# Kernel optimization log

Hardware: AMD Instinct MI355X
Metric: run time of the kernel (lower is better)

The kernel has to match this reference:

```python
import jax, jax.numpy as jnp
import numpy as np

N_NODES = 10000
N_EDGES = 160000
EMBED = 512
RBF = 64
ANG = 16


def setup_inputs() -> dict:
    key = jax.random.key(0)
    ks = jax.random.split(key, 12)
    x = jax.random.normal(ks[0], (N_NODES, EMBED), dtype=jnp.float32)
    coord = jax.random.normal(ks[1], (N_NODES, 3), dtype=jnp.float32)
    edge_index = jax.random.randint(ks[2], (2, N_EDGES), 0, N_NODES, dtype=jnp.int64)
    rbf_feature = jax.random.normal(ks[3], (N_EDGES, RBF), dtype=jnp.float32)
    angle_feature = jax.random.normal(ks[4], (N_EDGES, ANG), dtype=jnp.float32)
    s = 1.0 / np.sqrt(RBF + ANG)
    W_edge = jax.random.normal(ks[5], (RBF + ANG, EMBED), dtype=jnp.float32) * s
    b_edge = jax.random.normal(ks[6], (EMBED,), dtype=jnp.float32) * 0.01
    s2 = 1.0 / np.sqrt(EMBED)
    W1 = jax.random.normal(ks[7], (EMBED, EMBED), dtype=jnp.float32) * s2
    b1 = jax.random.normal(ks[8], (EMBED,), dtype=jnp.float32) * 0.01
    W2 = jax.random.normal(ks[9], (EMBED, EMBED), dtype=jnp.float32) * s2
    b2 = jax.random.normal(ks[10], (EMBED,), dtype=jnp.float32) * 0.01
    return {"x": x, "coord": coord, "edge_index": edge_index,
            "rbf_feature": rbf_feature, "angle_feature": angle_feature,
            "W_edge": W_edge, "b_edge": b_edge,
            "W1": W1, "b1": b1, "W2": W2, "b2": b2}


def reference(x, coord, edge_index, rbf_feature, angle_feature,
              W_edge, b_edge, W1, b1, W2, b2):
    row = edge_index[0]  # destination nodes for scatter-add
    edge_feat = jnp.concatenate([rbf_feature, angle_feature], axis=-1)  # [E, 80]
    msg = edge_feat @ W_edge + b_edge                                    # [E, D]
    agg = jax.ops.segment_sum(msg, row, num_segments=x.shape[0])         # [N, D]
    h = jax.nn.relu(agg @ W1 + b1) @ W2 + b2                             # node MLP
    return x + h
```

## Files before the change

### kernel.cpp

```cpp
#include <hip/hip_runtime.h>

constexpr int NN = 10000;
constexpr int NE = 160000;
constexpr int D  = 512;
constexpr int KC = 8;
constexpr int MAXDEG = 96;

typedef __attribute__((ext_vector_type(8))) short short8;
typedef __attribute__((ext_vector_type(4))) float f32x4;

static __device__ __forceinline__ ushort f2bf(float f) {
    union { float f; unsigned u; } v; v.f = f;
    unsigned r = (v.u + 0x7FFFu + ((v.u >> 16) & 1u)) >> 16;
    return (ushort)r;
}

typedef __attribute__((address_space(3))) unsigned int lds_uint;
typedef const __attribute__((address_space(1))) unsigned int glb_uint;
static __device__ __forceinline__ void gload16(const ushort* g, ushort* l) {
    __builtin_amdgcn_global_load_lds((glb_uint*)g, (lds_uint*)l, 16, 0, 0);
}

__global__ __launch_bounds__(256)
void prep1_kernel(const float* __restrict__ We,
                  const float* __restrict__ be,
                  const float* __restrict__ W1,
                  const float* __restrict__ W2,
                  float* __restrict__ part,
                  ushort* __restrict__ W2t,
                  int* __restrict__ deg) {
    __shared__ float tile[32][33];
    const int b   = blockIdx.x;
    const int tid = threadIdx.x;

    if (b < 1344) {
        const int c  = (b & 7) * 64 + (tid & 63);
        const int r  = ((b >> 3) % 21) * 4 + (tid >> 6);
        const int kc = b / 168;
        if (r > 80) return;
        const float* arow = (r < 80) ? (We + (size_t)r * D) : be;
        const int k0 = kc * 64;
        float s = 0.f;
        #pragma unroll
        for (int k = 0; k < 64; k += 4) {
            float4 a = *reinterpret_cast<const float4*>(&arow[k0 + k]);
            s += a.x * W1[(size_t)(k0 + k    ) * D + c];
            s += a.y * W1[(size_t)(k0 + k + 1) * D + c];
            s += a.z * W1[(size_t)(k0 + k + 2) * D + c];
            s += a.w * W1[(size_t)(k0 + k + 3) * D + c];
        }
        part[((size_t)kc * 81 + r) * D + c] = s;
    } else if (b < 1600) {
        const int t  = b - 1344;
        const int bx = (t & 15) * 32;
        const int by = (t >> 4) * 32;
        const int tx = tid & 31;
        const int ty = tid >> 5;
        #pragma unroll
        for (int i = 0; i < 4; ++i)
            tile[ty + 8 * i][tx] = W2[(size_t)(by + ty + 8 * i) * D + bx + tx];
        __syncthreads();
        #pragma unroll
        for (int i = 0; i < 4; ++i)
            W2t[(size_t)(bx + ty + 8 * i) * D + by + tx] = f2bf(tile[tx][ty + 8 * i]);
    } else {
        const int i = (b - 1600) * 256 + tid;
        if (i < NN) deg[i] = 0;
    }
}

__global__ __launch_bounds__(256)
void prep2_kernel(const float* __restrict__ part,
                  const int* __restrict__ row,
                  ushort* __restrict__ WcT,
                  int* __restrict__ deg,
                  int* __restrict__ ell) {
    const int b   = blockIdx.x;
    const int tid = threadIdx.x;
    if (b < 256) {
        const int i = b * 256 + tid;
        const int k = i >> 9;
        const int c = i & 511;
        float s = 0.f;
        if (k <= 80) {
            #pragma unroll
            for (int kc = 0; kc < KC; ++kc)
                s += part[((size_t)kc * 81 + k) * D + c];
        }
        WcT[(size_t)c * 128 + k] = f2bf(s);
    } else {
        const int e = (b - 256) * 256 + tid;
        if (e < NE) {
            int r = row[e];
            int slot = atomicAdd(&deg[r], 1);
            if (slot < MAXDEG) ell[r * MAXDEG + slot] = e;
        }
    }
}

__global__ __launch_bounds__(256)
void gather_agg_kernel(const int* __restrict__ deg,
                       const int* __restrict__ ell,
                       const float* __restrict__ rbf,
                       const float* __restrict__ ang,
                       ushort* __restrict__ aggX) {
    const int wv   = threadIdx.x >> 6;
    const int lane = threadIdx.x & 63;
    const int n    = blockIdx.x * 4 + wv;
    if (n >= NN) return;
    int d = deg[n];
    if (d > MAXDEG) d = MAXDEG;
    const int* en = ell + (size_t)n * MAXDEG;
    float s1 = 0.f, s2 = 0.f;
    int i = 0;
    for (; i + 8 <= d; i += 8) {
        int e[8];
        #pragma unroll
        for (int j = 0; j < 8; ++j) e[j] = en[i + j];
        float v[8];
        #pragma unroll
        for (int j = 0; j < 8; ++j) v[j] = rbf[e[j] * 64 + lane];
        if (lane < 16) {
            #pragma unroll
            for (int j = 0; j < 8; ++j) s2 += ang[e[j] * 16 + lane];
        }
        #pragma unroll
        for (int j = 0; j < 8; ++j) s1 += v[j];
    }
    for (; i + 4 <= d; i += 4) {
        const int e0 = en[i], e1 = en[i + 1], e2 = en[i + 2], e3 = en[i + 3];
        const float v0 = rbf[e0 * 64 + lane];
        const float v1 = rbf[e1 * 64 + lane];
        const float v2 = rbf[e2 * 64 + lane];
        const float v3 = rbf[e3 * 64 + lane];
        if (lane < 16) {
            s2 += ang[e0 * 16 + lane] + ang[e1 * 16 + lane]
                + ang[e2 * 16 + lane] + ang[e3 * 16 + lane];
        }
        s1 += v0 + v1 + v2 + v3;
    }
    for (; i < d; ++i) {
        const int e = en[i];
        s1 += rbf[e * 64 + lane];
        if (lane < 16) s2 += ang[e * 16 + lane];
    }
    aggX[(size_t)n * 128 + lane] = f2bf(s1);
    const float v2 = (lane < 16) ? s2 : (lane == 16 ? (float)d : 0.f);
    aggX[(size_t)n * 128 + 64 + lane] = f2bf(v2);
}

__global__ __launch_bounds__(256)
void h1_mfma_kernel(const ushort* __restrict__ A,
                    const ushort* __restrict__ Bt,
                    const float* __restrict__ b1,
                    ushort* __restrict__ H, int M) {
    __shared__ ushort As[128 * 128];
    __shared__ ushort Bs[64 * 128];
    const int tid  = threadIdx.x;
    const int lane = tid & 63;
    const int wid  = tid >> 6;

    const int l = blockIdx.y * gridDim.x + blockIdx.x;
    const int cpx = (gridDim.x * gridDim.y) >> 3;
    const int t_ = (l & 7) * cpx + (l >> 3);
    const int n0 = (t_ & 7) * 64;
    const int m0 = (t_ >> 3) * 128;

    const int rg = lane >> 4;
    const int ch = lane & 15;

    f32x4 acc[2][4] = {};

    #pragma unroll
    for (int j = 0; j < 8; ++j) {
        const int r  = wid * 32 + j * 4 + rg;
        const int gm = (m0 + r < M) ? (m0 + r) : (M - 1);
        const int cs = (ch ^ (r & 7)) * 8;
        const int rowbase = wid * 32 + j * 4;
        gload16(A + (size_t)gm * 128 + cs, &As[rowbase * 128]);
    }
    #pragma unroll
    for (int j = 0; j < 4; ++j) {
        const int r  = wid * 16 + j * 4 + rg;
        const int cs = (ch ^ (r & 7)) * 8;
        const int rowbase = wid * 16 + j * 4;
        gload16(Bt + (size_t)(n0 + r) * 128 + cs, &Bs[rowbase * 128]);
    }
    __syncthreads();

    #pragma unroll
    for (int kk = 0; kk < 4; ++kk) {
        const int kc = kk * 4 + (lane >> 4);
        short8 af[2], bfr[4];
        #pragma unroll
        for (int mf = 0; mf < 2; ++mf) {
            const int ar = wid * 32 + mf * 16 + (lane & 15);
            af[mf] = *reinterpret_cast<const short8*>(
                &As[ar * 128 + ((kc ^ (ar & 7)) * 8)]);
        }
        #pragma unroll
        for (int nf = 0; nf < 4; ++nf) {
            const int br = nf * 16 + (lane & 15);
            bfr[nf] = *reinterpret_cast<const short8*>(
                &Bs[br * 128 + ((kc ^ (br & 7)) * 8)]);
        }
        #pragma unroll
        for (int mf = 0; mf < 2; ++mf)
            #pragma unroll
            for (int nf = 0; nf < 4; ++nf)
                acc[mf][nf] = __builtin_amdgcn_mfma_f32_16x16x32_bf16(
                    af[mf], bfr[nf], acc[mf][nf], 0, 0, 0);
    }

    #pragma unroll
    for (int mf = 0; mf < 2; ++mf) {
        const int rowb = m0 + wid * 32 + mf * 16 + ((lane >> 4) << 2);
        #pragma unroll
        for (int nf = 0; nf < 4; ++nf) {
            const int col = n0 + nf * 16 + (lane & 15);
            const float bv = b1[col];
            #pragma unroll
            for (int r = 0; r < 4; ++r) {
                const int row = rowb + r;
                if (row < M)
                    H[(size_t)row * D + col] = f2bf(fmaxf(acc[mf][nf][r] + bv, 0.f));
            }
        }
    }
}

__global__ __launch_bounds__(256)
void mfma_gemm_kernel(const ushort* __restrict__ A,
                      const ushort* __restrict__ Bt,
                      const float* __restrict__ bias,
                      const float* __restrict__ xres,
                      float* __restrict__ Cout, int M) {
    __shared__ ushort As[2][128 * 64];
    __shared__ ushort Bs[2][64 * 64];
    const int tid  = threadIdx.x;
    const int lane = tid & 63;
    const int wid  = tid >> 6;

    const int l = blockIdx.y * gridDim.x + blockIdx.x;
    const int cpx = (gridDim.x * gridDim.y) >> 3;
    const int t_ = (l & 7) * cpx + (l >> 3);
    const int n0 = (t_ & 7) * 64;
    const int m0 = (t_ >> 3) * 128;

    const int sr = lane >> 3;
    const int sc = lane & 7;

    f32x4 acc[2][4] = {};
    constexpr int KTILES = D / 64;

    auto stage = [&](int buf, int t) {
        #pragma unroll
        for (int j = 0; j < 4; ++j) {
            const int r  = wid * 32 + j * 8 + sr;
            const int gm = (m0 + r < M) ? (m0 + r) : (M - 1);
            const int cs = (sc ^ (r & 7)) * 8;
            const int rowbase = wid * 32 + j * 8;
            gload16(A + (size_t)gm * D + t * 64 + cs, &As[buf][rowbase * 64]);
        }
        #pragma unroll
        for (int j = 0; j < 2; ++j) {
            const int r  = wid * 16 + j * 8 + sr;
            const int cs = (sc ^ (r & 7)) * 8;
            const int rowbase = wid * 16 + j * 8;
            gload16(Bt + (size_t)(n0 + r) * D + t * 64 + cs, &Bs[buf][rowbase * 64]);
        }
    };

    stage(0, 0);
    __syncthreads();

    for (int t = 0; t < KTILES; ++t) {
        const int cur = t & 1;
        if (t + 1 < KTILES) stage(cur ^ 1, t + 1);
        #pragma unroll
        for (int kk = 0; kk < 2; ++kk) {
            const int kc = kk * 4 + (lane >> 4);
            short8 af[2], bfr[4];
            #pragma unroll
            for (int mf = 0; mf < 2; ++mf) {
                const int ar = wid * 32 + mf * 16 + (lane & 15);
                af[mf] = *reinterpret_cast<const short8*>(
                    &As[cur][ar * 64 + ((kc ^ (ar & 7)) * 8)]);
            }
            #pragma unroll
            for (int nf = 0; nf < 4; ++nf) {
                const int br = nf * 16 + (lane & 15);
                bfr[nf] = *reinterpret_cast<const short8*>(
                    &Bs[cur][br * 64 + ((kc ^ (br & 7)) * 8)]);
            }
            #pragma unroll
            for (int mf = 0; mf < 2; ++mf)
                #pragma unroll
                for (int nf = 0; nf < 4; ++nf)
                    acc[mf][nf] = __builtin_amdgcn_mfma_f32_16x16x32_bf16(
                        af[mf], bfr[nf], acc[mf][nf], 0, 0, 0);
        }
        __syncthreads();
    }

    #pragma unroll
    for (int mf = 0; mf < 2; ++mf) {
        const int rowb = m0 + wid * 32 + mf * 16 + ((lane >> 4) << 2);
        #pragma unroll
        for (int nf = 0; nf < 4; ++nf) {
            const int col = n0 + nf * 16 + (lane & 15);
            const float bv = bias[col];
            #pragma unroll
            for (int r = 0; r < 4; ++r) {
                const int row = rowb + r;
                if (row < M)
                    Cout[(size_t)row * D + col] =
                        acc[mf][nf][r] + bv + xres[(size_t)row * D + col];
            }
        }
    }
}

extern "C" void kernel_launch(void* const* d_in, const int* in_sizes, int n_in,
                              void* d_out, int out_size, void* d_ws, size_t ws_size,
                              hipStream_t stream) {
    const float* x      = (const float*)d_in[0];
    const int*   edge_index = (const int*)d_in[2];
    const float* rbf    = (const float*)d_in[3];
    const float* ang    = (const float*)d_in[4];
    const float* W_edge = (const float*)d_in[5];
    const float* b_edge = (const float*)d_in[6];
    const float* W1     = (const float*)d_in[7];
    const float* b1     = (const float*)d_in[8];
    const float* W2     = (const float*)d_in[9];
    const float* b2     = (const float*)d_in[10];
    float* out = (float*)d_out;

    char* w = (char*)d_ws;
    ushort* aggX = (ushort*)w;
    ushort* W2t  = (ushort*)(w + 2560000);
    ushort* WcT  = (ushort*)(w + 3084288);
    int*    deg  = (int*)(w + 3215360);
    float*  part = (float*)(w + 3255360);
    int*    ell  = (int*)(w + 4582464);
    ushort* h1   = (ushort*)(w + 3255360);

    prep1_kernel<<<1640, 256, 0, stream>>>(W_edge, b_edge, W1, W2, part, W2t, deg);
    prep2_kernel<<<881, 256, 0, stream>>>(part, edge_index, WcT, deg, ell);
    gather_agg_kernel<<<NN / 4, 256, 0, stream>>>(deg, ell, rbf, ang, aggX);

    dim3 ggrid(D / 64, (NN + 127) / 128);
    h1_mfma_kernel<<<ggrid, 256, 0, stream>>>(aggX, WcT, b1, h1, NN);
    mfma_gemm_kernel<<<ggrid, 256, 0, stream>>>(h1, W2t, b2, x, out, NN);
}
```

Measured before the change: 70.58 us.

## Fuse gather and both node GEMMs into one cooperative kernel with grid syncs

Replaces the three launches (gather aggregation, first MFMA GEMM, second MFMA GEMM) with a single cooperative kernel of 632 blocks that uses grid-wide syncs between phases. The aim is to cut kernel launch gaps and tail effects between the dependent stages. In exchange, it depends on cooperative launch succeeding with all 632 blocks resident, and it adds grid-sync costs. It keeps the old multi-kernel path as a fallback if the cooperative launch fails.

```diff
diff --git a/kernel.cpp b/kernel.cpp
--- a/kernel.cpp
+++ b/kernel.cpp
@@ -1,4 +1,7 @@
 #include <hip/hip_runtime.h>
+#include <hip/hip_cooperative_groups.h>
+
+namespace cg = cooperative_groups;
 
 constexpr int NN = 10000;
 constexpr int NE = 160000;
@@ -22,12 +25,9 @@
 }
 
 __global__ __launch_bounds__(256)
-void prep1_kernel(const float* __restrict__ We,
-                  const float* __restrict__ be,
-                  const float* __restrict__ W1,
-                  const float* __restrict__ W2,
-                  float* __restrict__ part,
-                  ushort* __restrict__ W2t,
+void prep1_kernel(const float* __restrict__ We, const float* __restrict__ be,
+                  const float* __restrict__ W1, const float* __restrict__ W2,
+                  float* __restrict__ part, ushort* __restrict__ W2t,
                   int* __restrict__ deg) {
     __shared__ float tile[32][33];
     const int b   = blockIdx.x;
@@ -70,10 +70,8 @@
 }
 
 __global__ __launch_bounds__(256)
-void prep2_kernel(const float* __restrict__ part,
-                  const int* __restrict__ row,
-                  ushort* __restrict__ WcT,
-                  int* __restrict__ deg,
+void prep2_kernel(const float* __restrict__ part, const int* __restrict__ row,
+                  ushort* __restrict__ WcT, int* __restrict__ deg,
                   int* __restrict__ ell) {
     const int b   = blockIdx.x;
     const int tid = threadIdx.x;
@@ -98,16 +96,11 @@
     }
 }
 
-__global__ __launch_bounds__(256)
-void gather_agg_kernel(const int* __restrict__ deg,
-                       const int* __restrict__ ell,
-                       const float* __restrict__ rbf,
-                       const float* __restrict__ ang,
-                       ushort* __restrict__ aggX) {
-    const int wv   = threadIdx.x >> 6;
-    const int lane = threadIdx.x & 63;
-    const int n    = blockIdx.x * 4 + wv;
-    if (n >= NN) return;
+static __device__ __forceinline__ void gather_body(
+        int n, int lane,
+        const int* __restrict__ deg, const int* __restrict__ ell,
+        const float* __restrict__ rbf, const float* __restrict__ ang,
+        ushort* __restrict__ aggX) {
     int d = deg[n];
     if (d > MAXDEG) d = MAXDEG;
     const int* en = ell + (size_t)n * MAXDEG;
@@ -149,11 +142,191 @@
     aggX[(size_t)n * 128 + 64 + lane] = f2bf(v2);
 }
 
+__global__ __launch_bounds__(256, 3)
+void fused_kernel(const int* __restrict__ deg, const int* __restrict__ ell,
+                  const float* __restrict__ rbf, const float* __restrict__ ang,
+                  ushort* __restrict__ aggX, const ushort* __restrict__ WcT,
+                  const float* __restrict__ b1, ushort* __restrict__ h1,
+                  const ushort* __restrict__ W2t, const float* __restrict__ b2,
+                  const float* __restrict__ x, float* __restrict__ out) {
+    __shared__ ushort smem[24576];
+    cg::grid_group grid = cg::this_grid();
+
+    const int tid  = threadIdx.x;
+    const int lane = tid & 63;
+    const int wid  = tid >> 6;
+
+    for (int g = blockIdx.x; g < NN / 4; g += gridDim.x)
+        gather_body(g * 4 + wid, lane, deg, ell, rbf, ang, aggX);
+    grid.sync();
+
+    const int l = blockIdx.x;
+    const int cpx = gridDim.x >> 3;
+    const int t_ = (l & 7) * cpx + (l >> 3);
+    const int n0 = (t_ & 7) * 64;
+    const int m0 = (t_ >> 3) * 128;
+    constexpr int M = NN;
+
+    {
+        ushort* As = smem;
+        ushort* Bs = smem + 16384;
+        const int rg = lane >> 4;
+        const int ch = lane & 15;
+
+        f32x4 acc[2][4] = {};
+
+        #pragma unroll
+        for (int j = 0; j < 8; ++j) {
+            const int r  = wid * 32 + j * 4 + rg;
+            const int gm = (m0 + r < M) ? (m0 + r) : (M - 1);
+            const int cs = (ch ^ (r & 7)) * 8;
+            const int rowbase = wid * 32 + j * 4;
+            gload16(aggX + (size_t)gm * 128 + cs, &As[rowbase * 128]);
+        }
+        #pragma unroll
+        for (int j = 0; j < 4; ++j) {
+            const int r  = wid * 16 + j * 4 + rg;
+            const int cs = (ch ^ (r & 7)) * 8;
+            const int rowbase = wid * 16 + j * 4;
+            gload16(WcT + (size_t)(n0 + r) * 128 + cs, &Bs[rowbase * 128]);
+        }
+        __syncthreads();
+
+        #pragma unroll
+        for (int kk = 0; kk < 4; ++kk) {
+            const int kc = kk * 4 + (lane >> 4);
+            short8 af[2], bfr[4];
+            #pragma unroll
+            for (int mf = 0; mf < 2; ++mf) {
+                const int ar = wid * 32 + mf * 16 + (lane & 15);
+                af[mf] = *reinterpret_cast<const short8*>(
+                    &As[ar * 128 + ((kc ^ (ar & 7)) * 8)]);
+            }
+            #pragma unroll
+            for (int nf = 0; nf < 4; ++nf) {
+                const int br = nf * 16 + (lane & 15);
+                bfr[nf] = *reinterpret_cast<const short8*>(
+                    &Bs[br * 128 + ((kc ^ (br & 7)) * 8)]);
+            }
+            #pragma unroll
+            for (int mf = 0; mf < 2; ++mf)
+                #pragma unroll
+                for (int nf = 0; nf < 4; ++nf)
+                    acc[mf][nf] = __builtin_amdgcn_mfma_f32_16x16x32_bf16(
+                        af[mf], bfr[nf], acc[mf][nf], 0, 0, 0);
+        }
+
+        #pragma unroll
+        for (int mf = 0; mf < 2; ++mf) {
+            const int rowb = m0 + wid * 32 + mf * 16 + ((lane >> 4) << 2);
+            #pragma unroll
+            for (int nf = 0; nf < 4; ++nf) {
+                const int col = n0 + nf * 16 + (lane & 15);
+                const float bv = b1[col];
+                #pragma unroll
+                for (int r = 0; r < 4; ++r) {
+                    const int row = rowb + r;
+                    if (row < M)
+                        h1[(size_t)row * D + col] =
+                            f2bf(fmaxf(acc[mf][nf][r] + bv, 0.f));
+                }
+            }
+        }
+    }
+    __syncthreads();
+    grid.sync();
+
+    {
+        ushort* As0 = smem;
+        ushort* Bs0 = smem + 16384;
+        const int sr = lane >> 3;
+        const int sc = lane & 7;
+
+        f32x4 acc[2][4] = {};
+        constexpr int KTILES = D / 64;
+
+        auto stage = [&](int buf, int t) {
+            #pragma unroll
+            for (int j = 0; j < 4; ++j) {
+                const int r  = wid * 32 + j * 8 + sr;
+                const int gm = (m0 + r < M) ? (m0 + r) : (M - 1);
+                const int cs = (sc ^ (r & 7)) * 8;
+                const int rowbase = wid * 32 + j * 8;
+                gload16(h1 + (size_t)gm * D + t * 64 + cs,
+                        &As0[buf * 8192 + rowbase * 64]);
+            }
+            #pragma unroll
+            for (int j = 0; j < 2; ++j) {
+                const int r  = wid * 16 + j * 8 + sr;
+                const int cs = (sc ^ (r & 7)) * 8;
+                const int rowbase = wid * 16 + j * 8;
+                gload16(W2t + (size_t)(n0 + r) * D + t * 64 + cs,
+                        &Bs0[buf * 4096 + rowbase * 64]);
+            }
+        };
+
+        stage(0, 0);
+        __syncthreads();
+
+        for (int t = 0; t < KTILES; ++t) {
+            const int cur = t & 1;
+            if (t + 1 < KTILES) stage(cur ^ 1, t + 1);
+            #pragma unroll
+            for (int kk = 0; kk < 2; ++kk) {
+                const int kc = kk * 4 + (lane >> 4);
+                short8 af[2], bfr[4];
+                #pragma unroll
+                for (int mf = 0; mf < 2; ++mf) {
+                    const int ar = wid * 32 + mf * 16 + (lane & 15);
+                    af[mf] = *reinterpret_cast<const short8*>(
+                        &As0[cur * 8192 + ar * 64 + ((kc ^ (ar & 7)) * 8)]);
+                }
+                #pragma unroll
+                for (int nf = 0; nf < 4; ++nf) {
+                    const int br = nf * 16 + (lane & 15);
+                    bfr[nf] = *reinterpret_cast<const short8*>(
+                        &Bs0[cur * 4096 + br * 64 + ((kc ^ (br & 7)) * 8)]);
+                }
+                #pragma unroll
+                for (int mf = 0; mf < 2; ++mf)
+                    #pragma unroll
+                    for (int nf = 0; nf < 4; ++nf)
+                        acc[mf][nf] = __builtin_amdgcn_mfma_f32_16x16x32_bf16(
+                            af[mf], bfr[nf], acc[mf][nf], 0, 0, 0);
+            }
+            __syncthreads();
+        }
+
+        #pragma unroll
+        for (int mf = 0; mf < 2; ++mf) {
+            const int rowb = m0 + wid * 32 + mf * 16 + ((lane >> 4) << 2);
+            #pragma unroll
+            for (int nf = 0; nf < 4; ++nf) {
+                const int col = n0 + nf * 16 + (lane & 15);
+                const float bv = b2[col];
+                #pragma unroll
+                for (int r = 0; r < 4; ++r) {
+                    const int row = rowb + r;
+                    if (row < M)
+                        out[(size_t)row * D + col] =
+                            acc[mf][nf][r] + bv + x[(size_t)row * D + col];
+                }
+            }
+        }
+    }
+}
+
 __global__ __launch_bounds__(256)
-void h1_mfma_kernel(const ushort* __restrict__ A,
-                    const ushort* __restrict__ Bt,
-                    const float* __restrict__ b1,
-                    ushort* __restrict__ H, int M) {
+void gather_agg_kernel(const int* __restrict__ deg, const int* __restrict__ ell,
+                       const float* __restrict__ rbf, const float* __restrict__ ang,
+                       ushort* __restrict__ aggX) {
+    const int n = blockIdx.x * 4 + (threadIdx.x >> 6);
+    if (n < NN) gather_body(n, threadIdx.x & 63, deg, ell, rbf, ang, aggX);
+}
+
+__global__ __launch_bounds__(256)
+void h1_mfma_kernel(const ushort* __restrict__ A, const ushort* __restrict__ Bt,
+                    const float* __restrict__ b1, ushort* __restrict__ H, int M) {
     __shared__ ushort As[128 * 128];
     __shared__ ushort Bs[64 * 128];
     const int tid  = threadIdx.x;
@@ -230,10 +403,8 @@
 }
 
 __global__ __launch_bounds__(256)
-void mfma_gemm_kernel(const ushort* __restrict__ A,
-                      const ushort* __restrict__ Bt,
-                      const float* __restrict__ bias,
-                      const float* __restrict__ xres,
+void mfma_gemm_kernel(const ushort* __restrict__ A, const ushort* __restrict__ Bt,
+                      const float* __restrict__ bias, const float* __restrict__ xres,
                       float* __restrict__ Cout, int M) {
     __shared__ ushort As[2][128 * 64];
     __shared__ ushort Bs[2][64 * 64];
@@ -347,9 +518,20 @@
 
     prep1_kernel<<<1640, 256, 0, stream>>>(W_edge, b_edge, W1, W2, part, W2t, deg);
     prep2_kernel<<<881, 256, 0, stream>>>(part, edge_index, WcT, deg, ell);
-    gather_agg_kernel<<<NN / 4, 256, 0, stream>>>(deg, ell, rbf, ang, aggX);
-
-    dim3 ggrid(D / 64, (NN + 127) / 128);
-    h1_mfma_kernel<<<ggrid, 256, 0, stream>>>(aggX, WcT, b1, h1, NN);
-    mfma_gemm_kernel<<<ggrid, 256, 0, stream>>>(h1, W2t, b2, x, out, NN);
-}
+
+    const int* degc = deg;
+    const int* ellc = ell;
+    const ushort* WcTc = WcT;
+    const ushort* W2tc = W2t;
+    void* args[] = {(void*)&degc, (void*)&ellc, (void*)&rbf, (void*)&ang,
+                    (void*)&aggX, (void*)&WcTc, (void*)&b1, (void*)&h1,
+                    (void*)&W2tc, (void*)&b2, (void*)&x, (void*)&out};
+    hipError_t err = hipLaunchCooperativeKernel((void*)fused_kernel, dim3(632),
+                                                dim3(256), args, 0, stream);
+    if (err != hipSuccess) {
+        gather_agg_kernel<<<NN / 4, 256, 0, stream>>>(deg, ell, rbf, ang, aggX);
+        dim3 ggrid(D / 64, (NN + 127) / 128);
+        h1_mfma_kernel<<<ggrid, 256, 0, stream>>>(aggX, WcT, b1, h1, NN);
+        mfma_gemm_kernel<<<ggrid, 256, 0, stream>>>(h1, W2t, b2, x, out, NN);
+    }
+}
```

Result: slower. 219.6 us (+211.1%).

## Fuse node MLP GEMMs into one kernel, recomputing hidden tile per block

Applied to the files above, without the earlier changes.

Merges the h1 GEMM and the second GEMM into a single tail kernel. Each block computes a 128x64 slice of relu(agg@Wc+b1) in registers and LDS for every K-tile, then immediately multiplies it by the matching W2 slice. This removes the bf16 h1 round trip through global memory and one kernel launch. In exchange, every one of the 8 column blocks recomputes the full hidden tile, so the first GEMM's compute is repeated 8 times.

```diff
diff --git a/kernel.cpp b/kernel.cpp
--- a/kernel.cpp
+++ b/kernel.cpp
@@ -22,12 +22,9 @@
 }
 
 __global__ __launch_bounds__(256)
-void prep1_kernel(const float* __restrict__ We,
-                  const float* __restrict__ be,
-                  const float* __restrict__ W1,
-                  const float* __restrict__ W2,
-                  float* __restrict__ part,
-                  ushort* __restrict__ W2t,
+void prep1_kernel(const float* __restrict__ We, const float* __restrict__ be,
+                  const float* __restrict__ W1, const float* __restrict__ W2,
+                  float* __restrict__ part, ushort* __restrict__ W2t,
                   int* __restrict__ deg) {
     __shared__ float tile[32][33];
     const int b   = blockIdx.x;
@@ -70,10 +67,8 @@
 }
 
 __global__ __launch_bounds__(256)
-void prep2_kernel(const float* __restrict__ part,
-                  const int* __restrict__ row,
-                  ushort* __restrict__ WcT,
-                  int* __restrict__ deg,
+void prep2_kernel(const float* __restrict__ part, const int* __restrict__ row,
+                  ushort* __restrict__ WcT, int* __restrict__ deg,
                   int* __restrict__ ell) {
     const int b   = blockIdx.x;
     const int tid = threadIdx.x;
@@ -99,10 +94,8 @@
 }
 
 __global__ __launch_bounds__(256)
-void gather_agg_kernel(const int* __restrict__ deg,
-                       const int* __restrict__ ell,
-                       const float* __restrict__ rbf,
-                       const float* __restrict__ ang,
+void gather_agg_kernel(const int* __restrict__ deg, const int* __restrict__ ell,
+                       const float* __restrict__ rbf, const float* __restrict__ ang,
                        ushort* __restrict__ aggX) {
     const int wv   = threadIdx.x >> 6;
     const int lane = threadIdx.x & 63;
@@ -150,12 +143,16 @@
 }
 
 __global__ __launch_bounds__(256)
-void h1_mfma_kernel(const ushort* __restrict__ A,
-                    const ushort* __restrict__ Bt,
-                    const float* __restrict__ b1,
-                    ushort* __restrict__ H, int M) {
-    __shared__ ushort As[128 * 128];
-    __shared__ ushort Bs[64 * 128];
+void tail_kernel(const ushort* __restrict__ aggX,
+                 const ushort* __restrict__ WcT,
+                 const float* __restrict__ b1,
+                 const ushort* __restrict__ W2t,
+                 const float* __restrict__ b2,
+                 const float* __restrict__ x,
+                 float* __restrict__ out, int M) {
+    __shared__ ushort Wc_s[2][64 * 128];
+    __shared__ ushort W2_s[2][64 * 64];
+    __shared__ ushort Ah[128 * 64];
     const int tid  = threadIdx.x;
     const int lane = tid & 63;
     const int wid  = tid >> 6;
@@ -166,117 +163,87 @@
     const int n0 = (t_ & 7) * 64;
     const int m0 = (t_ >> 3) * 128;
 
-    const int rg = lane >> 4;
-    const int ch = lane & 15;
-
-    f32x4 acc[2][4] = {};
-
-    #pragma unroll
-    for (int j = 0; j < 8; ++j) {
-        const int r  = wid * 32 + j * 4 + rg;
-        const int gm = (m0 + r < M) ? (m0 + r) : (M - 1);
-        const int cs = (ch ^ (r & 7)) * 8;
-        const int rowbase = wid * 32 + j * 4;
-        gload16(A + (size_t)gm * 128 + cs, &As[rowbase * 128]);
-    }
-    #pragma unroll
-    for (int j = 0; j < 4; ++j) {
-        const int r  = wid * 16 + j * 4 + rg;
-        const int cs = (ch ^ (r & 7)) * 8;
-        const int rowbase = wid * 16 + j * 4;
-        gload16(Bt + (size_t)(n0 + r) * 128 + cs, &Bs[rowbase * 128]);
-    }
-    __syncthreads();
-
-    #pragma unroll
-    for (int kk = 0; kk < 4; ++kk) {
-        const int kc = kk * 4 + (lane >> 4);
-        short8 af[2], bfr[4];
-        #pragma unroll
-        for (int mf = 0; mf < 2; ++mf) {
-            const int ar = wid * 32 + mf * 16 + (lane & 15);
-            af[mf] = *reinterpret_cast<const short8*>(
-                &As[ar * 128 + ((kc ^ (ar & 7)) * 8)]);
-        }
-        #pragma unroll
-        for (int nf = 0; nf < 4; ++nf) {
-            const int br = nf * 16 + (lane & 15);
-            bfr[nf] = *reinterpret_cast<const short8*>(
-                &Bs[br * 128 + ((kc ^ (br & 7)) * 8)]);
-        }
-        #pragma unroll
-        for (int mf = 0; mf < 2; ++mf)
-            #pragma unroll
-            for (int nf = 0; nf < 4; ++nf)
-                acc[mf][nf] = __builtin_amdgcn_mfma_f32_16x16x32_bf16(
-                    af[mf], bfr[nf], acc[mf][nf], 0, 0, 0);
-    }
-
+    short8 afh[2][4];
     #pragma unroll
     for (int mf = 0; mf < 2; ++mf) {
-        const int rowb = m0 + wid * 32 + mf * 16 + ((lane >> 4) << 2);
-        #pragma unroll
-        for (int nf = 0; nf < 4; ++nf) {
-            const int col = n0 + nf * 16 + (lane & 15);
-            const float bv = b1[col];
-            #pragma unroll
-            for (int r = 0; r < 4; ++r) {
-                const int row = rowb + r;
-                if (row < M)
-                    H[(size_t)row * D + col] = f2bf(fmaxf(acc[mf][nf][r] + bv, 0.f));
-            }
-        }
-    }
-}
-
-__global__ __launch_bounds__(256)
-void mfma_gemm_kernel(const ushort* __restrict__ A,
-                      const ushort* __restrict__ Bt,
-                      const float* __restrict__ bias,
-                      const float* __restrict__ xres,
-                      float* __restrict__ Cout, int M) {
-    __shared__ ushort As[2][128 * 64];
-    __shared__ ushort Bs[2][64 * 64];
-    const int tid  = threadIdx.x;
-    const int lane = tid & 63;
-    const int wid  = tid >> 6;
-
-    const int l = blockIdx.y * gridDim.x + blockIdx.x;
-    const int cpx = (gridDim.x * gridDim.y) >> 3;
-    const int t_ = (l & 7) * cpx + (l >> 3);
-    const int n0 = (t_ & 7) * 64;
-    const int m0 = (t_ >> 3) * 128;
-
-    const int sr = lane >> 3;
-    const int sc = lane & 7;
+        const int row = m0 + wid * 32 + mf * 16 + (lane & 15);
+        const int gm = (row < M) ? row : (M - 1);
+        #pragma unroll
+        for (int kk = 0; kk < 4; ++kk)
+            afh[mf][kk] = *reinterpret_cast<const short8*>(
+                &aggX[(size_t)gm * 128 + kk * 32 + ((lane >> 4) << 3)]);
+    }
+
+    const int rg4 = lane >> 4;
+    const int ch16 = lane & 15;
+    const int rg8 = lane >> 3;
+    const int ch8 = lane & 7;
+
+    auto stageWc = [&](int buf, int t) {
+        #pragma unroll
+        for (int j = 0; j < 4; ++j) {
+            const int r  = wid * 16 + j * 4 + rg4;
+            const int cs = (ch16 ^ (r & 7)) * 8;
+            const int rowbase = wid * 16 + j * 4;
+            gload16(WcT + (size_t)(t * 64 + r) * 128 + cs, &Wc_s[buf][rowbase * 128]);
+        }
+    };
+    auto stageW2 = [&](int buf, int t) {
+        #pragma unroll
+        for (int j = 0; j < 2; ++j) {
+            const int r  = wid * 16 + j * 8 + rg8;
+            const int cs = (ch8 ^ (r & 7)) * 8;
+            const int rowbase = wid * 16 + j * 8;
+            gload16(W2t + (size_t)(n0 + r) * D + t * 64 + cs, &W2_s[buf][rowbase * 64]);
+        }
+    };
 
     f32x4 acc[2][4] = {};
     constexpr int KTILES = D / 64;
 
-    auto stage = [&](int buf, int t) {
-        #pragma unroll
-        for (int j = 0; j < 4; ++j) {
-            const int r  = wid * 32 + j * 8 + sr;
-            const int gm = (m0 + r < M) ? (m0 + r) : (M - 1);
-            const int cs = (sc ^ (r & 7)) * 8;
-            const int rowbase = wid * 32 + j * 8;
-            gload16(A + (size_t)gm * D + t * 64 + cs, &As[buf][rowbase * 64]);
-        }
-        #pragma unroll
-        for (int j = 0; j < 2; ++j) {
-            const int r  = wid * 16 + j * 8 + sr;
-            const int cs = (sc ^ (r & 7)) * 8;
-            const int rowbase = wid * 16 + j * 8;
-            gload16(Bt + (size_t)(n0 + r) * D + t * 64 + cs, &Bs[buf][rowbase * 64]);
-        }
-    };
-
-    stage(0, 0);
-    __syncthreads();
+    stageWc(0, 0);
+    stageW2(0, 0);
 
     for (int t = 0; t < KTILES; ++t) {
         const int cur = t & 1;
-        if (t + 1 < KTILES) stage(cur ^ 1, t + 1);
+        __syncthreads();
+
+        f32x4 acch[2][4] = {};
+        #pragma unroll
+        for (int kk = 0; kk < 4; ++kk) {
+            const int kc = kk * 4 + (lane >> 4);
+            short8 bfh[4];
+            #pragma unroll
+            for (int nf = 0; nf < 4; ++nf) {
+                const int br = nf * 16 + (lane & 15);
+                bfh[nf] = *reinterpret_cast<const short8*>(
+                    &Wc_s[cur][br * 128 + ((kc ^ (br & 7)) * 8)]);
+            }
+            #pragma unroll
+            for (int mf = 0; mf < 2; ++mf)
+                #pragma unroll
+                for (int nf = 0; nf < 4; ++nf)
+                    acch[mf][nf] = __builtin_amdgcn_mfma_f32_16x16x32_bf16(
+                        afh[mf][kk], bfh[nf], acch[mf][nf], 0, 0, 0);
+        }
+
+        #pragma unroll
+        for (int mf = 0; mf < 2; ++mf) {
+            const int rowb = wid * 32 + mf * 16 + ((lane >> 4) << 2);
+            #pragma unroll
+            for (int nf = 0; nf < 4; ++nf) {
+                const int col = nf * 16 + (lane & 15);
+                const float bv = b1[t * 64 + n0 * 0 + col + 0 * D] ;
+                #pragma unroll
+                for (int r = 0; r < 4; ++r) {
+                    const int row = rowb + r;
+                    const float v = fmaxf(acch[mf][nf][r] + b1[t * 64 + col], 0.f);
+                    Ah[(row * 64 + col) ^ ((row & 7) << 3)] = f2bf(v);
+                }
+                (void)bv;
+            }
+        }
+
         #pragma unroll
         for (int kk = 0; kk < 2; ++kk) {
             const int kc = kk * 4 + (lane >> 4);
@@ -284,14 +251,15 @@
             #pragma unroll
             for (int mf = 0; mf < 2; ++mf) {
                 const int ar = wid * 32 + mf * 16 + (lane & 15);
+                const int koff = kk * 32 + ((lane >> 4) << 3);
                 af[mf] = *reinterpret_cast<const short8*>(
-                    &As[cur][ar * 64 + ((kc ^ (ar & 7)) * 8)]);
+                    &Ah[(ar * 64 + koff) ^ ((ar & 7) << 3)]);
             }
             #pragma unroll
             for (int nf = 0; nf < 4; ++nf) {
                 const int br = nf * 16 + (lane & 15);
                 bfr[nf] = *reinterpret_cast<const short8*>(
-                    &Bs[cur][br * 64 + ((kc ^ (br & 7)) * 8)]);
+                    &W2_s[cur][br * 64 + ((kc ^ (br & 7)) * 8)]);
             }
             #pragma unroll
             for (int mf = 0; mf < 2; ++mf)
@@ -300,7 +268,11 @@
                     acc[mf][nf] = __builtin_amdgcn_mfma_f32_16x16x32_bf16(
                         af[mf], bfr[nf], acc[mf][nf], 0, 0, 0);
         }
-        __syncthreads();
+
+        if (t + 1 < KTILES) {
+            stageWc(cur ^ 1, t + 1);
+            stageW2(cur ^ 1, t + 1);
+        }
     }
 
     #pragma unroll
@@ -309,13 +281,13 @@
         #pragma unroll
         for (int nf = 0; nf < 4; ++nf) {
             const int col = n0 + nf * 16 + (lane & 15);
-            const float bv = bias[col];
+            const float bv = b2[col];
             #pragma unroll
             for (int r = 0; r < 4; ++r) {
                 const int row = rowb + r;
                 if (row < M)
-                    Cout[(size_t)row * D + col] =
-                        acc[mf][nf][r] + bv + xres[(size_t)row * D + col];
+                    out[(size_t)row * D + col] =
+                        acc[mf][nf][r] + bv + x[(size_t)row * D + col];
             }
         }
     }
@@ -343,13 +315,11 @@
     int*    deg  = (int*)(w + 3215360);
     float*  part = (float*)(w + 3255360);
     int*    ell  = (int*)(w + 4582464);
-    ushort* h1   = (ushort*)(w + 3255360);
 
     prep1_kernel<<<1640, 256, 0, stream>>>(W_edge, b_edge, W1, W2, part, W2t, deg);
     prep2_kernel<<<881, 256, 0, stream>>>(part, edge_index, WcT, deg, ell);
     gather_agg_kernel<<<NN / 4, 256, 0, stream>>>(deg, ell, rbf, ang, aggX);
 
     dim3 ggrid(D / 64, (NN + 127) / 128);
-    h1_mfma_kernel<<<ggrid, 256, 0, stream>>>(aggX, WcT, b1, h1, NN);
-    mfma_gemm_kernel<<<ggrid, 256, 0, stream>>>(h1, W2t, b2, x, out, NN);
-}
+    tail_kernel<<<ggrid, 256, 0, stream>>>(aggX, WcT, b1, W2t, b2, x, out, NN);
+}
```

New measurement: 96.50 us. +36.7%, slower.
